# Performance work log

Measured on AMD Instinct MI355X. Metric: run time of the kernel, lower is better.

The kernel has to match this reference:

```python
import jax, jax.numpy as jnp
import numpy as np

DIM = 1024
NUM_HEADS = 16
HEAD_DIM = DIM // NUM_HEADS
ROPE_BASE = 10000.0


def rope_freqs(t):
    # [t, head_dim]: standard rotary angles, duplicated across both halves
    inv_freq = 1.0 / (ROPE_BASE ** (jnp.arange(0, HEAD_DIM, 2, dtype=jnp.float32) / HEAD_DIM))
    angles = jnp.arange(t, dtype=jnp.float32)[:, None] * inv_freq[None, :]  # [t, hd/2]
    return jnp.concatenate([angles, angles], axis=-1)  # [t, hd]


def rotate_half(x):
    x1, x2 = jnp.split(x, 2, axis=-1)
    return jnp.concatenate([-x2, x1], axis=-1)


def apply_rope(freqs, x):
    # freqs: [t, hd] broadcast to x: [b, h, t, hd]
    cos = jnp.cos(freqs)[None, None]
    sin = jnp.sin(freqs)[None, None]
    return x * cos + rotate_half(x) * sin


def setup_inputs() -> dict:
    key = jax.random.key(0)
    k1, k2, k3 = jax.random.split(key, 3)
    b, t = 2, 2048
    x = jax.random.normal(k1, (b, t, DIM), dtype=jnp.float32)
    Wqkv = jax.random.normal(k2, (DIM, 3 * DIM), dtype=jnp.float32) * (DIM ** -0.5)
    Wout = jax.random.normal(k3, (DIM, DIM), dtype=jnp.float32) * (DIM ** -0.5)
    bout = jnp.zeros((DIM,), dtype=jnp.float32)
    return {"x": x, "Wqkv": Wqkv, "Wout": Wout, "bout": bout}


def reference(x, Wqkv, Wout, bout):
    b, t, c = x.shape
    scale = HEAD_DIM ** -0.5
    qkv = x @ Wqkv  # [b, t, 3c]
    q, k, v = jnp.split(qkv, 3, axis=-1)
    def to_heads(a):
        return a.reshape(b, t, NUM_HEADS, HEAD_DIM).transpose(0, 2, 1, 3)  # [b,h,t,hd]
    q, k, v = to_heads(q), to_heads(k), to_heads(v)
    freqs = rope_freqs(t)
    q = apply_rope(freqs, q)
    k = apply_rope(freqs, k)
    attn = jnp.einsum('bhqd,bhkd->bhqk', q, k) * scale
    attn = jax.nn.softmax(attn, axis=-1)
    out = jnp.einsum('bhqk,bhkd->bhqd', attn, v)
    out = out.transpose(0, 2, 1, 3).reshape(b, t, c)
    return out @ Wout + bout
```

## Files before the change

### kernel.cpp

```cpp
#include <hip/hip_runtime.h>
#include <hip/hip_bf16.h>
#include <cstdint>

#define TT 2048
#define HD 64
#define NH 16
#define CDIM 1024
#define N3 3072
#define BT 4096
#define QSCALE 0.18033688011112042f

using bf16 = __hip_bfloat16;
typedef __attribute__((ext_vector_type(4))) float f32x4;
typedef __attribute__((ext_vector_type(8))) short short8;
typedef __attribute__((ext_vector_type(8))) __bf16 bf16x8v;

__device__ __forceinline__ short f2bbits(float f) {
  __hip_bfloat16 h = __float2bfloat16(f);
  return __builtin_bit_cast(short, h);
}

__device__ __forceinline__ f32x4 mfma_bf16(short8 a, short8 b, f32x4 c) {
  return __builtin_amdgcn_mfma_f32_16x16x32_bf16(
      __builtin_bit_cast(bf16x8v, a), __builtin_bit_cast(bf16x8v, b), c, 0, 0, 0);
}

__device__ __forceinline__ void gll16(const void* g, void* l) {
  __builtin_amdgcn_global_load_lds(
      (const __attribute__((address_space(1))) void*)g,
      (__attribute__((address_space(3))) void*)l, 16, 0, 0);
}

__device__ __forceinline__ float exp2_fast(float x) {
  float r;
  asm("v_exp_f32 %0, %1" : "=v"(r) : "v"(x));
  return r;
}

__device__ __forceinline__ uint32_t pkbf16(float lo, float hi) {
  uint32_t lw = (uint32_t)(uint16_t)f2bbits(lo);
  uint32_t hw = (uint32_t)(uint16_t)f2bbits(hi);
  return (hw << 16) | lw;
}


__global__ __launch_bounds__(256) void cvt_f32_to_bf16(const float* __restrict__ in,
                                                       bf16* __restrict__ out, int n) {
  int idx = (blockIdx.x * 256 + threadIdx.x) * 8;
  if (idx >= n) return;
  float4 a = *(const float4*)(in + idx);
  float4 b = *(const float4*)(in + idx + 4);
  short8 o;
  o[0] = f2bbits(a.x); o[1] = f2bbits(a.y); o[2] = f2bbits(a.z); o[3] = f2bbits(a.w);
  o[4] = f2bbits(b.x); o[5] = f2bbits(b.y); o[6] = f2bbits(b.z); o[7] = f2bbits(b.w);
  *(short8*)(out + idx) = o;
}

__global__ __launch_bounds__(256) void transpose_to_bf16(const float* __restrict__ in,
                                                         bf16* __restrict__ out,
                                                         int R, int C) {
  __shared__ float tile[32][33];
  int c0 = blockIdx.x * 32, r0 = blockIdx.y * 32;
  int tx = threadIdx.x, ty = threadIdx.y;
#pragma unroll
  for (int i = 0; i < 32; i += 8)
    tile[ty + i][tx] = in[(size_t)(r0 + ty + i) * C + c0 + tx];
  __syncthreads();
#pragma unroll
  for (int i = 0; i < 32; i += 8)
    out[(size_t)(c0 + ty + i) * R + r0 + tx] = __float2bfloat16(tile[tx][ty + i]);
}

__global__ __launch_bounds__(256) void rope_table(float* __restrict__ cost,
                                                  float* __restrict__ sint) {
  int idx = blockIdx.x * 256 + threadIdx.x;
  int t = idx >> 5, i = idx & 31;
  double inv = exp(-(double)i / 32.0 * log(10000.0));
  double a = (double)t * inv;
  cost[idx] = (float)cos(a);
  sint[idx] = (float)sin(a);
}


__device__ __forceinline__ void gemm_core(const bf16* __restrict__ A, const bf16* __restrict__ Bt,
                                          int K, int m0, int n0, f32x4 acc[4][4],
                                          bf16* As, bf16* Bs) {
  int tid = threadIdx.x;
  int w = tid >> 6, l = tid & 63;
  int wm = (w >> 1) * 64, wn = (w & 1) * 64;
  for (int kt = 0; kt < K; kt += 64) {
#pragma unroll
    for (int it = 0; it < 4; ++it) {
      int ci = it * 256 + tid;
      int r = ci >> 3, cc = ci & 7;
      int sc = cc ^ (r & 7);
      gll16(A + (size_t)(m0 + r) * K + kt + sc * 8, As + (it * 256 + w * 64) * 8);
      gll16(Bt + (size_t)(n0 + r) * K + kt + sc * 8, Bs + (it * 256 + w * 64) * 8);
    }
    __syncthreads();
#pragma unroll
    for (int c = 0; c < 2; ++c) {
      short8 af[4], bfr[4];
#pragma unroll
      for (int i = 0; i < 4; ++i) {
        int row = wm + i * 16 + (l & 15);
        int colE = c * 32 + (l >> 4) * 8;
        af[i] = *(const short8*)(As + row * 64 + (colE ^ ((row & 7) << 3)));
      }
#pragma unroll
      for (int j = 0; j < 4; ++j) {
        int row = wn + j * 16 + (l & 15);
        int colE = c * 32 + (l >> 4) * 8;
        bfr[j] = *(const short8*)(Bs + row * 64 + (colE ^ ((row & 7) << 3)));
      }
#pragma unroll
      for (int i = 0; i < 4; ++i)
#pragma unroll
        for (int j = 0; j < 4; ++j)
          acc[i][j] = mfma_bf16(af[i], bfr[j], acc[i][j]);
    }
    __syncthreads();
  }
}

__global__ __launch_bounds__(256) void qkv_gemm(const bf16* __restrict__ xb,
                                                const bf16* __restrict__ WqkvT,
                                                const float* __restrict__ cost,
                                                const float* __restrict__ sint,
                                                bf16* __restrict__ Qb, bf16* __restrict__ Kb,
                                                bf16* __restrict__ VTb) {
  __shared__ bf16 Sh[2 * 128 * 64];
  bf16* As = Sh;
  bf16* Bs = Sh + 128 * 64;
  int m0 = blockIdx.y * 128, n0 = blockIdx.x * 128;
  f32x4 acc[4][4] = {};
  gemm_core(xb, WqkvT, CDIM, m0, n0, acc, As, Bs);
  int tid = threadIdx.x, w = tid >> 6, l = tid & 63;
  int wm = (w >> 1) * 64, wn = (w & 1) * 64;
  int which = n0 >> 10;
  if (which < 2) {
    int h = ((n0 + wn) & 1023) >> 6;
    bf16* Out = which == 0 ? Qb : Kb;
    float sc = (which == 0) ? QSCALE : 1.0f;
#pragma unroll
    for (int i = 0; i < 4; ++i)
#pragma unroll
      for (int r = 0; r < 4; ++r) {
        int m = m0 + wm + i * 16 + (l >> 4) * 4 + r;
        int b = m >> 11, t = m & 2047;
        size_t base = (((size_t)(b * NH + h)) * TT + t) * HD;
#pragma unroll
        for (int j = 0; j < 2; ++j) {
          int ii = j * 16 + (l & 15);
          float c = cost[t * 32 + ii], s = sint[t * 32 + ii];
          float x1 = acc[i][j][r], x2 = acc[i][j + 2][r];
          Out[base + ii]      = __float2bfloat16((x1 * c - x2 * s) * sc);
          Out[base + ii + 32] = __float2bfloat16((x2 * c + x1 * s) * sc);
        }
      }
  } else {
    const int BP = 136;
    int hb = (n0 & 1023) >> 6;
    int b = m0 >> 11, t0 = m0 & 2047;
#pragma unroll
    for (int p = 0; p < 2; ++p) {
      if ((w & 1) == p) {
#pragma unroll
        for (int i = 0; i < 4; ++i)
#pragma unroll
          for (int j = 0; j < 4; ++j)
#pragma unroll
            for (int r = 0; r < 4; ++r) {
              int dloc = j * 16 + (l & 15);
              int mloc = wm + i * 16 + (l >> 4) * 4 + r;
              Sh[dloc * BP + mloc] = __float2bfloat16(acc[i][j][r]);
            }
      }
      __syncthreads();
      {
        int dloc = tid >> 2, tch = (tid & 3) * 32;
        bf16* dst = VTb + (((size_t)(b * NH + hb + p)) * HD + dloc) * TT + t0 + tch;
        const bf16* srcb = Sh + dloc * BP + tch;
#pragma unroll
        for (int k2 = 0; k2 < 4; ++k2)
          *(uint4*)(dst + k2 * 8) = *(const uint4*)(srcb + k2 * 8);
      }
      __syncthreads();
    }
  }
}

__global__ __launch_bounds__(256) void out_gemm(const bf16* __restrict__ Ob,
                                                const bf16* __restrict__ WoutT,
                                                const float* __restrict__ bout,
                                                float* __restrict__ out) {
  __shared__ bf16 As[128 * 64];
  __shared__ bf16 Bs[128 * 64];
  int m0 = blockIdx.y * 128, n0 = blockIdx.x * 128;
  f32x4 acc[4][4] = {};
  gemm_core(Ob, WoutT, CDIM, m0, n0, acc, As, Bs);
  int tid = threadIdx.x, w = tid >> 6, l = tid & 63;
  int wm = (w >> 1) * 64, wn = (w & 1) * 64;
#pragma unroll
  for (int i = 0; i < 4; ++i)
#pragma unroll
    for (int j = 0; j < 4; ++j)
#pragma unroll
      for (int r = 0; r < 4; ++r) {
        int m = m0 + wm + i * 16 + (l >> 4) * 4 + r;
        int n = n0 + wn + j * 16 + (l & 15);
        out[(size_t)m * CDIM + n] = acc[i][j][r] + bout[n];
      }
}

#define VP 68
__global__ __launch_bounds__(256) void attn(const bf16* __restrict__ Q,
                                            const bf16* __restrict__ K,
                                            const bf16* __restrict__ VT,
                                            bf16* __restrict__ O) {
  __shared__ bf16 Ks[64 * 64];
  __shared__ bf16 Vs[64 * VP];
  int bh = blockIdx.y, q0 = blockIdx.x * 64;
  int tid = threadIdx.x, w = tid >> 6, l = tid & 63;
  int g = l >> 4, qi = l & 15;

  const bf16* Qg = Q + ((size_t)bh * TT + q0) * HD;
  const bf16* Kg = K + (size_t)bh * TT * HD;
  const bf16* Vg = VT + (size_t)bh * TT * HD;

#pragma unroll
  for (int it = 0; it < 2; ++it) {
    int ci = it * 256 + tid, r = ci >> 3, cc = ci & 7;
    gll16(Qg + (size_t)r * HD + (cc ^ (r & 7)) * 8, &Ks[0] + (it * 256 + w * 64) * 8);
  }
  __syncthreads();
  short8 aq[2];
#pragma unroll
  for (int c = 0; c < 2; ++c) {
    int row = w * 16 + qi;
    int colE = c * 32 + g * 8;
    aq[c] = *(const short8*)(&Ks[row * 64 + (colE ^ ((row & 7) << 3))]);
  }
  __syncthreads();

  f32x4 oacc[4] = {};
  float lsum = 0.f;

  for (int kt = 0; kt < TT; kt += 64) {
    uint4 vreg[2];
#pragma unroll
    for (int it = 0; it < 2; ++it) {
      int ci = it * 256 + tid, r = ci >> 3, cc = ci & 7;
      gll16(Kg + (size_t)(kt + r) * HD + (cc ^ (r & 7)) * 8, &Ks[0] + (it * 256 + w * 64) * 8);
      vreg[it] = *(const uint4*)(Vg + (size_t)r * TT + kt + cc * 8);
    }
#pragma unroll
    for (int it = 0; it < 2; ++it) {
      int ci = it * 256 + tid, r = ci >> 3, cc = ci & 7;
      *(uint4*)(&Vs[r * VP + cc * 8]) = vreg[it];
    }
    __syncthreads();

    f32x4 s[4] = {};
    __builtin_amdgcn_s_setprio(1);
#pragma unroll
    for (int kn = 0; kn < 4; ++kn) {
#pragma unroll
      for (int c = 0; c < 2; ++c) {
        int row = kn * 16 + qi;
        int colE = c * 32 + g * 8;
        short8 kf = *(const short8*)(&Ks[row * 64 + (colE ^ ((row & 7) << 3))]);
        s[kn] = mfma_bf16(kf, aq[c], s[kn]);
      }
    }
    __builtin_amdgcn_s_setprio(0);

    uint32_t wlo[4], whi[4];
#pragma unroll
    for (int kn = 0; kn < 4; ++kn) {
      float p0 = exp2_fast(s[kn][0]);
      float p1 = exp2_fast(s[kn][1]);
      float p2 = exp2_fast(s[kn][2]);
      float p3 = exp2_fast(s[kn][3]);
      lsum += (p0 + p1) + (p2 + p3);
      wlo[kn] = pkbf16(p0, p1);
      whi[kn] = pkbf16(p2, p3);
    }

    __builtin_amdgcn_s_setprio(1);
#pragma unroll
    for (int c = 0; c < 2; ++c) {
      union { short8 s8; uint32_t u[4]; } pa;
      pa.u[0] = wlo[2 * c];     pa.u[1] = whi[2 * c];
      pa.u[2] = wlo[2 * c + 1]; pa.u[3] = whi[2 * c + 1];
#pragma unroll
      for (int dn = 0; dn < 4; ++dn) {
        int row = dn * 16 + qi;
        int e1 = c * 32 + g * 4;
        uint2 v0 = *(const uint2*)(&Vs[row * VP + e1]);
        uint2 v1 = *(const uint2*)(&Vs[row * VP + e1 + 16]);
        union { short8 s8; uint32_t u[4]; } vb;
        vb.u[0] = v0.x; vb.u[1] = v0.y; vb.u[2] = v1.x; vb.u[3] = v1.y;
        oacc[dn] = mfma_bf16(pa.s8, vb.s8, oacc[dn]);
      }
    }
    __builtin_amdgcn_s_setprio(0);
    __syncthreads();
  }

  float tot = lsum;
  tot += __shfl_xor(tot, 16, 64);
  tot += __shfl_xor(tot, 32, 64);

  int b = bh >> 4, hh = bh & 15;
#pragma unroll
  for (int r = 0; r < 4; ++r) {
    float lq = __shfl(tot, g * 4 + r, 64);
    float inv = 1.0f / lq;
    int t = q0 + w * 16 + g * 4 + r;
    bf16* Orow = O + ((size_t)(b * TT + t)) * CDIM + hh * HD;
#pragma unroll
    for (int dn = 0; dn < 4; ++dn)
      Orow[dn * 16 + qi] = __float2bfloat16(oacc[dn][r] * inv);
  }
}


extern "C" void kernel_launch(void* const* d_in, const int* in_sizes, int n_in,
                              void* d_out, int out_size, void* d_ws, size_t ws_size,
                              hipStream_t stream) {
  const float* x    = (const float*)d_in[0];
  const float* Wqkv = (const float*)d_in[1];
  const float* Wout = (const float*)d_in[2];
  const float* bout = (const float*)d_in[3];
  float* out = (float*)d_out;

  char* ws = (char*)d_ws;
  bf16* xb     = (bf16*)(ws);
  bf16* WqkvT  = (bf16*)(ws + 8388608);
  bf16* WoutT  = (bf16*)(ws + 14680064);
  bf16* Qb     = (bf16*)(ws + 16777216);
  bf16* Kb     = (bf16*)(ws + 25165824);
  bf16* VTb    = (bf16*)(ws + 41943040);
  float* cost  = (float*)(ws + 50331648);
  float* sint  = (float*)(ws + 50593792);
  bf16* Ob     = xb;

  cvt_f32_to_bf16<<<2048, 256, 0, stream>>>(x, xb, BT * CDIM);
  transpose_to_bf16<<<dim3(96, 32), dim3(32, 8), 0, stream>>>(Wqkv, WqkvT, CDIM, N3);
  transpose_to_bf16<<<dim3(32, 32), dim3(32, 8), 0, stream>>>(Wout, WoutT, CDIM, CDIM);
  rope_table<<<256, 256, 0, stream>>>(cost, sint);
  qkv_gemm<<<dim3(24, 32), 256, 0, stream>>>(xb, WqkvT, cost, sint, Qb, Kb, VTb);
  attn<<<dim3(32, 32), 256, 0, stream>>>(Qb, Kb, VTb, Ob);
  out_gemm<<<dim3(8, 32), 256, 0, stream>>>(Ob, WoutT, bout, out);
}
```

Measured before the change: 140.3 us.

## Fuse prep kernels into one launch and process two KV tiles per attention sync

The four preprocessing kernels (x convert, two weight transposes, rope table) are merged into a single block-indexed launch to cut launch overhead and let the pieces run concurrently. The attention loop now loads two 64-key K/V tiles into doubled LDS buffers per iteration, halving the number of barriers and batching global loads. This doubles attention LDS use and register pressure for V staging, which may lower occupancy. The transpose body relies on a __syncthreads inside a divergent branch, which is uniform per block here.

Result: faster. 134.1 us (-4.4%).

```diff
diff --git a/kernel.cpp b/kernel.cpp
--- a/kernel.cpp
+++ b/kernel.cpp
@@ -44,24 +44,11 @@
 }
 
 
-__global__ __launch_bounds__(256) void cvt_f32_to_bf16(const float* __restrict__ in,
-                                                       bf16* __restrict__ out, int n) {
-  int idx = (blockIdx.x * 256 + threadIdx.x) * 8;
-  if (idx >= n) return;
-  float4 a = *(const float4*)(in + idx);
-  float4 b = *(const float4*)(in + idx + 4);
-  short8 o;
-  o[0] = f2bbits(a.x); o[1] = f2bbits(a.y); o[2] = f2bbits(a.z); o[3] = f2bbits(a.w);
-  o[4] = f2bbits(b.x); o[5] = f2bbits(b.y); o[6] = f2bbits(b.z); o[7] = f2bbits(b.w);
-  *(short8*)(out + idx) = o;
-}
-
-__global__ __launch_bounds__(256) void transpose_to_bf16(const float* __restrict__ in,
-                                                         bf16* __restrict__ out,
-                                                         int R, int C) {
-  __shared__ float tile[32][33];
-  int c0 = blockIdx.x * 32, r0 = blockIdx.y * 32;
-  int tx = threadIdx.x, ty = threadIdx.y;
+__device__ __forceinline__ void transpose_body(const float* __restrict__ in,
+                                               bf16* __restrict__ out, int R, int C,
+                                               int bx, int by, int tx, int ty,
+                                               float (*tile)[33]) {
+  int c0 = bx * 32, r0 = by * 32;
 #pragma unroll
   for (int i = 0; i < 32; i += 8)
     tile[ty + i][tx] = in[(size_t)(r0 + ty + i) * C + c0 + tx];
@@ -71,14 +58,34 @@
     out[(size_t)(c0 + ty + i) * R + r0 + tx] = __float2bfloat16(tile[tx][ty + i]);
 }
 
-__global__ __launch_bounds__(256) void rope_table(float* __restrict__ cost,
-                                                  float* __restrict__ sint) {
-  int idx = blockIdx.x * 256 + threadIdx.x;
-  int t = idx >> 5, i = idx & 31;
-  double inv = exp(-(double)i / 32.0 * log(10000.0));
-  double a = (double)t * inv;
-  cost[idx] = (float)cos(a);
-  sint[idx] = (float)sin(a);
+__global__ __launch_bounds__(256) void prep(const float* __restrict__ x, bf16* __restrict__ xb,
+                                            const float* __restrict__ Wqkv, bf16* __restrict__ WqkvT,
+                                            const float* __restrict__ Wout, bf16* __restrict__ WoutT,
+                                            float* __restrict__ cost, float* __restrict__ sint) {
+  __shared__ float tile[32][33];
+  int bid = blockIdx.x, tid = threadIdx.x;
+  if (bid < 2048) {
+    int idx = (bid * 256 + tid) * 8;
+    float4 a = *(const float4*)(x + idx);
+    float4 b = *(const float4*)(x + idx + 4);
+    short8 o;
+    o[0] = f2bbits(a.x); o[1] = f2bbits(a.y); o[2] = f2bbits(a.z); o[3] = f2bbits(a.w);
+    o[4] = f2bbits(b.x); o[5] = f2bbits(b.y); o[6] = f2bbits(b.z); o[7] = f2bbits(b.w);
+    *(short8*)(xb + idx) = o;
+  } else if (bid < 5120) {
+    int id = bid - 2048;
+    transpose_body(Wqkv, WqkvT, CDIM, N3, id % 96, id / 96, tid & 31, tid >> 5, tile);
+  } else if (bid < 6144) {
+    int id = bid - 5120;
+    transpose_body(Wout, WoutT, CDIM, CDIM, id & 31, id >> 5, tid & 31, tid >> 5, tile);
+  } else {
+    int idx = (bid - 6144) * 256 + tid;
+    int t = idx >> 5, i = idx & 31;
+    double inv = exp(-(double)i / 32.0 * log(10000.0));
+    double a = (double)t * inv;
+    cost[idx] = (float)cos(a);
+    sint[idx] = (float)sin(a);
+  }
 }
 
 
@@ -218,8 +225,8 @@
                                             const bf16* __restrict__ K,
                                             const bf16* __restrict__ VT,
                                             bf16* __restrict__ O) {
-  __shared__ bf16 Ks[64 * 64];
-  __shared__ bf16 Vs[64 * VP];
+  __shared__ bf16 Ks[2][64 * 64];
+  __shared__ bf16 Vs[2][64 * VP];
   int bh = blockIdx.y, q0 = blockIdx.x * 64;
   int tid = threadIdx.x, w = tid >> 6, l = tid & 63;
   int g = l >> 4, qi = l & 15;
@@ -231,7 +238,7 @@
 #pragma unroll
   for (int it = 0; it < 2; ++it) {
     int ci = it * 256 + tid, r = ci >> 3, cc = ci & 7;
-    gll16(Qg + (size_t)r * HD + (cc ^ (r & 7)) * 8, &Ks[0] + (it * 256 + w * 64) * 8);
+    gll16(Qg + (size_t)r * HD + (cc ^ (r & 7)) * 8, &Ks[0][0] + (it * 256 + w * 64) * 8);
   }
   __syncthreads();
   short8 aq[2];
@@ -239,72 +246,80 @@
   for (int c = 0; c < 2; ++c) {
     int row = w * 16 + qi;
     int colE = c * 32 + g * 8;
-    aq[c] = *(const short8*)(&Ks[row * 64 + (colE ^ ((row & 7) << 3))]);
+    aq[c] = *(const short8*)(&Ks[0][row * 64 + (colE ^ ((row & 7) << 3))]);
   }
   __syncthreads();
 
   f32x4 oacc[4] = {};
   float lsum = 0.f;
 
-  for (int kt = 0; kt < TT; kt += 64) {
-    uint4 vreg[2];
-#pragma unroll
-    for (int it = 0; it < 2; ++it) {
-      int ci = it * 256 + tid, r = ci >> 3, cc = ci & 7;
-      gll16(Kg + (size_t)(kt + r) * HD + (cc ^ (r & 7)) * 8, &Ks[0] + (it * 256 + w * 64) * 8);
-      vreg[it] = *(const uint4*)(Vg + (size_t)r * TT + kt + cc * 8);
+  for (int kt = 0; kt < TT; kt += 128) {
+    uint4 vreg[2][2];
+#pragma unroll
+    for (int sub = 0; sub < 2; ++sub)
+#pragma unroll
+      for (int it = 0; it < 2; ++it) {
+        int ci = it * 256 + tid, r = ci >> 3, cc = ci & 7;
+        gll16(Kg + (size_t)(kt + sub * 64 + r) * HD + (cc ^ (r & 7)) * 8,
+              &Ks[sub][0] + (it * 256 + w * 64) * 8);
+        vreg[sub][it] = *(const uint4*)(Vg + (size_t)r * TT + kt + sub * 64 + cc * 8);
+      }
+#pragma unroll
+    for (int sub = 0; sub < 2; ++sub)
+#pragma unroll
+      for (int it = 0; it < 2; ++it) {
+        int ci = it * 256 + tid, r = ci >> 3, cc = ci & 7;
+        *(uint4*)(&Vs[sub][r * VP + cc * 8]) = vreg[sub][it];
+      }
+    __syncthreads();
+
+#pragma unroll
+    for (int sub = 0; sub < 2; ++sub) {
+      f32x4 s[4] = {};
+      __builtin_amdgcn_s_setprio(1);
+#pragma unroll
+      for (int kn = 0; kn < 4; ++kn) {
+#pragma unroll
+        for (int c = 0; c < 2; ++c) {
+          int row = kn * 16 + qi;
+          int colE = c * 32 + g * 8;
+          short8 kf = *(const short8*)(&Ks[sub][row * 64 + (colE ^ ((row & 7) << 3))]);
+          s[kn] = mfma_bf16(kf, aq[c], s[kn]);
+        }
+      }
+      __builtin_amdgcn_s_setprio(0);
+
+      uint32_t wlo[4], whi[4];
+#pragma unroll
+      for (int kn = 0; kn < 4; ++kn) {
+        float p0 = exp2_fast(s[kn][0]);
+        float p1 = exp2_fast(s[kn][1]);
+        float p2 = exp2_fast(s[kn][2]);
+        float p3 = exp2_fast(s[kn][3]);
+        lsum += (p0 + p1) + (p2 + p3);
+        wlo[kn] = pkbf16(p0, p1);
+        whi[kn] = pkbf16(p2, p3);
+      }
+
+      __builtin_amdgcn_s_setprio(1);
+#pragma unroll
+      for (int c = 0; c < 2; ++c) {
+        union { short8 s8; uint32_t u[4]; } pa;
+        pa.u[0] = wlo[2 * c];     pa.u[1] = whi[2 * c];
+        pa.u[2] = wlo[2 * c + 1]; pa.u[3] = whi[2 * c + 1];
+#pragma unroll
+        for (int dn = 0; dn < 4; ++dn) {
+          int row = dn * 16 + qi;
+          int e1 = c * 32 + g * 4;
+          uint2 v0 = *(const uint2*)(&Vs[sub][row * VP + e1]);
+          uint2 v1 = *(const uint2*)(&Vs[sub][row * VP + e1 + 16]);
+          union { short8 s8; uint32_t u[4]; } vb;
+          vb.u[0] = v0.x; vb.u[1] = v0.y; vb.u[2] = v1.x; vb.u[3] = v1.y;
+          oacc[dn] = mfma_bf16(pa.s8, vb.s8, oacc[dn]);
+        }
+      }
+      __builtin_amdgcn_s_setprio(0);
     }
-#pragma unroll
-    for (int it = 0; it < 2; ++it) {
-      int ci = it * 256 + tid, r = ci >> 3, cc = ci & 7;
-      *(uint4*)(&Vs[r * VP + cc * 8]) = vreg[it];
-    }
-    __syncthreads();
-
-    f32x4 s[4] = {};
-    __builtin_amdgcn_s_setprio(1);
-#pragma unroll
-    for (int kn = 0; kn < 4; ++kn) {
-#pragma unroll
-      for (int c = 0; c < 2; ++c) {
-        int row = kn * 16 + qi;
-        int colE = c * 32 + g * 8;
-        short8 kf = *(const short8*)(&Ks[row * 64 + (colE ^ ((row & 7) << 3))]);
-        s[kn] = mfma_bf16(kf, aq[c], s[kn]);
-      }
-    }
-    __builtin_amdgcn_s_setprio(0);
-
-    uint32_t wlo[4], whi[4];
-#pragma unroll
-    for (int kn = 0; kn < 4; ++kn) {
-      float p0 = exp2_fast(s[kn][0]);
-      float p1 = exp2_fast(s[kn][1]);
-      float p2 = exp2_fast(s[kn][2]);
-      float p3 = exp2_fast(s[kn][3]);
-      lsum += (p0 + p1) + (p2 + p3);
-      wlo[kn] = pkbf16(p0, p1);
-      whi[kn] = pkbf16(p2, p3);
-    }
-
-    __builtin_amdgcn_s_setprio(1);
-#pragma unroll
-    for (int c = 0; c < 2; ++c) {
-      union { short8 s8; uint32_t u[4]; } pa;
-      pa.u[0] = wlo[2 * c];     pa.u[1] = whi[2 * c];
-      pa.u[2] = wlo[2 * c + 1]; pa.u[3] = whi[2 * c + 1];
-#pragma unroll
-      for (int dn = 0; dn < 4; ++dn) {
-        int row = dn * 16 + qi;
-        int e1 = c * 32 + g * 4;
-        uint2 v0 = *(const uint2*)(&Vs[row * VP + e1]);
-        uint2 v1 = *(const uint2*)(&Vs[row * VP + e1 + 16]);
-        union { short8 s8; uint32_t u[4]; } vb;
-        vb.u[0] = v0.x; vb.u[1] = v0.y; vb.u[2] = v1.x; vb.u[3] = v1.y;
-        oacc[dn] = mfma_bf16(pa.s8, vb.s8, oacc[dn]);
-      }
-    }
-    __builtin_amdgcn_s_setprio(0);
     __syncthreads();
   }
 
@@ -346,10 +361,7 @@
   float* sint  = (float*)(ws + 50593792);
   bf16* Ob     = xb;
 
-  cvt_f32_to_bf16<<<2048, 256, 0, stream>>>(x, xb, BT * CDIM);
-  transpose_to_bf16<<<dim3(96, 32), dim3(32, 8), 0, stream>>>(Wqkv, WqkvT, CDIM, N3);
-  transpose_to_bf16<<<dim3(32, 32), dim3(32, 8), 0, stream>>>(Wout, WoutT, CDIM, CDIM);
-  rope_table<<<256, 256, 0, stream>>>(cost, sint);
+  prep<<<6400, 256, 0, stream>>>(x, xb, Wqkv, WqkvT, Wout, WoutT, cost, sint);
   qkv_gemm<<<dim3(24, 32), 256, 0, stream>>>(xb, WqkvT, cost, sint, Qb, Kb, VTb);
   attn<<<dim3(32, 32), 256, 0, stream>>>(Qb, Kb, VTb, Ob);
   out_gemm<<<dim3(8, 32), 256, 0, stream>>>(Ob, WoutT, bout, out);
```
